# Performance work log

Measured on AMD Instinct MI355X. Metric: run time of the kernel, lower is better.

The kernel has to match this reference:

```python
import jax, jax.numpy as jnp
import numpy as np

D_MODEL = 2048
NUM_HEADS = 16
D_H = D_MODEL // NUM_HEADS
D_LATENT = 512
B, S = 2, 2048


def setup_inputs() -> dict:
    key = jax.random.key(0)
    ks = jax.random.split(key, 10)
    sd = lambda fan_in: 1.0 / np.sqrt(fan_in)
    x = jax.random.normal(ks[0], (B, S, D_MODEL), dtype=jnp.float32)
    # weights stored as [in, out] so y = x @ W + b (same math as nn.Linear)
    w_latent = jax.random.uniform(ks[1], (D_MODEL, D_LATENT), jnp.float32, -sd(D_MODEL), sd(D_MODEL))
    b_latent = jax.random.uniform(ks[2], (D_LATENT,), jnp.float32, -sd(D_MODEL), sd(D_MODEL))
    w_q = jax.random.uniform(ks[3], (D_MODEL, D_MODEL), jnp.float32, -sd(D_MODEL), sd(D_MODEL))
    b_q = jax.random.uniform(ks[4], (D_MODEL,), jnp.float32, -sd(D_MODEL), sd(D_MODEL))
    # per-head K/V projections batched into [H, d_latent, d_h]
    w_k = jax.random.uniform(ks[5], (NUM_HEADS, D_LATENT, D_H), jnp.float32, -sd(D_LATENT), sd(D_LATENT))
    b_k = jax.random.uniform(ks[6], (NUM_HEADS, D_H), jnp.float32, -sd(D_LATENT), sd(D_LATENT))
    w_v = jax.random.uniform(ks[7], (NUM_HEADS, D_LATENT, D_H), jnp.float32, -sd(D_LATENT), sd(D_LATENT))
    b_v = jax.random.uniform(ks[8], (NUM_HEADS, D_H), jnp.float32, -sd(D_LATENT), sd(D_LATENT))
    w_o = jax.random.uniform(ks[9], (D_MODEL, D_MODEL), jnp.float32, -sd(D_MODEL), sd(D_MODEL))
    b_o = jnp.zeros((D_MODEL,), jnp.float32)
    return {"x": x, "w_latent": w_latent, "b_latent": b_latent, "w_q": w_q, "b_q": b_q,
            "w_k": w_k, "b_k": b_k, "w_v": w_v, "b_v": b_v, "w_o": w_o, "b_o": b_o}


def reference(x, w_latent, b_latent, w_q, b_q, w_k, b_k, w_v, b_v, w_o, b_o):
    batch, seq, d = x.shape
    # latent KV compression: [B,S,d_latent]
    z = x @ w_latent + b_latent
    # queries: [B,H,S,d_h]
    q = (x @ w_q + b_q).reshape(batch, seq, NUM_HEADS, D_H).transpose(0, 2, 1, 3)
    # per-head K/V projections fused into one batched GEMM: [B,H,S,d_h]
    k = jnp.einsum('bsl,hld->bhsd', z, w_k) + b_k[None, :, None, :]
    v = jnp.einsum('bsl,hld->bhsd', z, w_v) + b_v[None, :, None, :]
    attn = jnp.einsum('bhqd,bhkd->bhqk', q, k) / np.sqrt(D_H).astype(np.float32)
    attn = jax.nn.softmax(attn, axis=-1)
    out = jnp.einsum('bhqk,bhkd->bhqd', attn, v)          # [B,H,S,d_h]
    out = out.transpose(0, 2, 1, 3).reshape(batch, seq, d)  # [B,S,D]
    return out @ w_o + b_o
```

## Files before the change

### kernel.cpp

```cpp
#include <hip/hip_runtime.h>
#include <hip/hip_bf16.h>

#define H_ATT   16
#define DH      128
#define DMODEL  2048
#define DLAT    512
#define NB      2
#define SEQ     2048
#define MROWS   (NB * SEQ)
#define NQZ     (DMODEL + DLAT)
#define NKV     (2 * DMODEL)

#define SCL2 0.12751744f

typedef __bf16          bf16x8_t __attribute__((ext_vector_type(8)));
typedef float           f32x4_t  __attribute__((ext_vector_type(4)));
typedef unsigned short  u16x4_t  __attribute__((ext_vector_type(4)));

#if __has_builtin(__builtin_amdgcn_exp2f)
#define EXP2F(x) __builtin_amdgcn_exp2f(x)
#else
#define EXP2F(x) exp2f(x)
#endif

__device__ __forceinline__ unsigned short f2bf_u16(float f) {
  union { __bf16 b; unsigned short u; } cv; cv.b = (__bf16)f; return cv.u;
}

__device__ __forceinline__ void async_copy16(const __bf16* g, __bf16* l) {
  __builtin_amdgcn_global_load_lds(
      (const __attribute__((address_space(1))) unsigned int*)g,
      (__attribute__((address_space(3))) unsigned int*)l, 16, 0, 0);
}

#define NB_CAST 8192
#define NB_WQ   4096
#define NB_WL   1024
#define NB_WK   1024
#define NB_WV   1024
#define NB_WO   4096
#define NB_BIAS 26
#define NB_PREP (NB_CAST + NB_WQ + NB_WL + NB_WK + NB_WV + NB_WO + NB_BIAS)

__global__ void prep(const float* __restrict__ x,
                     const float* __restrict__ w_q, const float* __restrict__ w_latent,
                     const float* __restrict__ w_k, const float* __restrict__ w_v,
                     const float* __restrict__ w_o,
                     const float* __restrict__ b_q, const float* __restrict__ b_lat,
                     const float* __restrict__ b_k, const float* __restrict__ b_v,
                     __bf16* __restrict__ xb, __bf16* __restrict__ wqzt,
                     __bf16* __restrict__ wkvt, __bf16* __restrict__ wot,
                     float* __restrict__ bqz, float* __restrict__ bkv) {
  __shared__ float tile[32][33];
  int bi = blockIdx.x;
  int t  = threadIdx.x;

  if (bi < NB_CAST) {
    int i = bi * 256 + t;
    float4 v = ((const float4*)x)[i];
    ushort4 o;
    o.x = f2bf_u16(v.x); o.y = f2bf_u16(v.y); o.z = f2bf_u16(v.z); o.w = f2bf_u16(v.w);
    ((ushort4*)xb)[i] = o;
    return;
  }
  bi -= NB_CAST;

  const float* in = nullptr; __bf16* out = nullptr;
  int R = 0, C = 0, bx = 0, by = 0; float scale = 1.f;
  if (bi < NB_WQ) {
    in = w_q; out = wqzt; R = DMODEL; C = DMODEL; scale = SCL2;
    bx = bi & 63; by = bi >> 6;
  } else if ((bi -= NB_WQ) < NB_WL) {
    in = w_latent; out = wqzt + (size_t)DMODEL * DMODEL; R = DMODEL; C = DLAT;
    bx = bi & 15; by = bi >> 4;
  } else if ((bi -= NB_WL) < NB_WK) {
    int h = bi >> 6, rem = bi & 63;
    in = w_k + (size_t)h * DLAT * DH; out = wkvt + (size_t)h * DH * DLAT;
    R = DLAT; C = DH; bx = rem & 3; by = rem >> 2;
  } else if ((bi -= NB_WK) < NB_WV) {
    int h = bi >> 6, rem = bi & 63;
    in = w_v + (size_t)h * DLAT * DH;
    out = wkvt + (size_t)DMODEL * DLAT + (size_t)h * DH * DLAT;
    R = DLAT; C = DH; bx = rem & 3; by = rem >> 2;
  } else if ((bi -= NB_WV) < NB_WO) {
    in = w_o; out = wot; R = DMODEL; C = DMODEL;
    bx = bi & 63; by = bi >> 6;
  } else {
    bi -= NB_WO;
    int idx = bi * 256 + t;
    if (idx < DMODEL)                bqz[idx] = b_q[idx] * SCL2;
    else if (idx < NQZ)              bqz[idx] = b_lat[idx - DMODEL];
    else if (idx < NQZ + DMODEL)     bkv[idx - NQZ] = b_k[idx - NQZ];
    else if (idx < NQZ + NKV)        bkv[idx - NQZ] = b_v[idx - NQZ - DMODEL];
    return;
  }

  int tx = t & 31, ty = t >> 5;
  const float* ip = in + (size_t)(by * 32) * C + bx * 32;
  #pragma unroll
  for (int i = 0; i < 4; ++i)
    tile[ty + i * 8][tx] = ip[(size_t)(ty + i * 8) * C + tx];
  __syncthreads();
  __bf16* op = out + (size_t)(bx * 32) * R + by * 32;
  #pragma unroll
  for (int i = 0; i < 4; ++i)
    op[(size_t)(ty + i * 8) * R + tx] = (__bf16)(tile[tx][ty + i * 8] * scale);
}

#define BM 128
#define BN 128
#define BK 32

__device__ __forceinline__ void storec(float*  p, float v) { *p = v; }
__device__ __forceinline__ void storec(__bf16* p, float v) { *p = (__bf16)v; }

template <typename OutT, bool KVDUAL>
__global__ __launch_bounds__(256, 2)
void gemm_bt(const __bf16* __restrict__ A, const __bf16* __restrict__ Bt,
             const float* __restrict__ bias, OutT* __restrict__ C,
             __bf16* __restrict__ Cvt,
             int M, int N, int K, int lda, int ldc) {
  __shared__ __align__(16) __bf16 As[BM * BK];
  __shared__ __align__(16) __bf16 Bs[BN * BK];
  const int t    = threadIdx.x;
  const int wave = t >> 6, lane = t & 63;
  const int quad = lane >> 4, l16 = lane & 15;
  const int wm = (wave >> 1) * 64, wn = (wave & 1) * 64;
  const int row0 = blockIdx.y * BM, col0 = blockIdx.x * BN;
  const int srow = t >> 2, skc = t & 3;

  const __bf16* Ag  = A  + (size_t)(row0 + srow)      * lda + skc * 8;
  const __bf16* Ag2 = A  + (size_t)(row0 + srow + 64) * lda + skc * 8;
  const __bf16* Bg  = Bt + (size_t)(col0 + srow)      * K   + skc * 8;
  const __bf16* Bg2 = Bt + (size_t)(col0 + srow + 64) * K   + skc * 8;
  __bf16* Al  = As + t * 8;
  __bf16* Al2 = As + 2048 + t * 8;
  __bf16* Bl  = Bs + t * 8;
  __bf16* Bl2 = Bs + 2048 + t * 8;

  f32x4_t acc[4][4] = {};

  for (int k0 = 0; k0 < K; k0 += BK) {
    async_copy16(Ag  + k0, Al);
    async_copy16(Ag2 + k0, Al2);
    async_copy16(Bg  + k0, Bl);
    async_copy16(Bg2 + k0, Bl2);
    __syncthreads();
    bf16x8_t af[4], bfr[4];
    #pragma unroll
    for (int i = 0; i < 4; ++i)
      af[i] = *(const bf16x8_t*)(As + (wm + i * 16 + l16) * BK + quad * 8);
    #pragma unroll
    for (int j = 0; j < 4; ++j)
      bfr[j] = *(const bf16x8_t*)(Bs + (wn + j * 16 + l16) * BK + quad * 8);
    #pragma unroll
    for (int i = 0; i < 4; ++i)
      #pragma unroll
      for (int j = 0; j < 4; ++j)
        acc[i][j] = __builtin_amdgcn_mfma_f32_16x16x32_bf16(af[i], bfr[j], acc[i][j], 0, 0, 0);
    __syncthreads();
  }

  const bool vmode = KVDUAL && (col0 >= DMODEL);
  #pragma unroll
  for (int j = 0; j < 4; ++j) {
    int col = col0 + wn + j * 16 + l16;
    float bj = bias[col];
    #pragma unroll
    for (int i = 0; i < 4; ++i) {
      int row = row0 + wm + i * 16 + quad * 4;
      if (vmode) {
        u16x4_t pw;
        #pragma unroll
        for (int r = 0; r < 4; ++r) pw[r] = f2bf_u16(acc[i][j][r] + bj);
        size_t bb = (size_t)(row >> 11);
        int s = row & (SEQ - 1);
        *(u16x4_t*)(Cvt + bb * ((size_t)DMODEL * SEQ) + (size_t)(col - DMODEL) * SEQ + s) = pw;
      } else {
        #pragma unroll
        for (int r = 0; r < 4; ++r)
          storec(&C[(size_t)(row + r) * ldc + col], acc[i][j][r] + bj);
      }
    }
  }
}

#define TQ 128
#define TK 64

__global__ __launch_bounds__(256, 2)
void mla_attn(const __bf16* __restrict__ Qm, const __bf16* __restrict__ Km,
              const __bf16* __restrict__ Vtg, __bf16* __restrict__ Om) {
  __shared__ __align__(16) __bf16 Kls[16 * 512];
  __shared__ __align__(16) __bf16 Vls[2][16 * 512];
  __shared__ __align__(16) __bf16 Ps [16 * 512];
  __shared__ float Lbuf[2][TQ];

  const int t    = threadIdx.x;
  const int wave = t >> 6, lane = t & 63;
  const int quad = lane >> 4, l16 = lane & 15;
  const int wq = wave >> 1, wk = wave & 1, wd = wave & 1;
  const int lin  = blockIdx.x;
  const int xcd  = lin & 7, slot = lin >> 3;
  const int hb   = xcd * 4 + (slot >> 4);
  const int b    = hb >> 4, h = hb & 15;
  const int q0   = (slot & 15) * TQ;
  const size_t kbase  = (size_t)b * SEQ * DMODEL + (size_t)h * DH;
  const size_t vtbase = ((size_t)b * DMODEL + (size_t)h * DH) * SEQ;
  const size_t obase  = (size_t)b * SEQ * DMODEL + (size_t)h * DH;

  bf16x8_t qf[4][4];
  #pragma unroll
  for (int nt = 0; nt < 4; ++nt) {
    const __bf16* qp = Qm + ((size_t)b * SEQ + q0 + wq * 64 + nt * 16 + l16) * NQZ
                       + (size_t)h * DH + quad * 8;
    #pragma unroll
    for (int kc = 0; kc < 4; ++kc)
      qf[nt][kc] = *(const bf16x8_t*)(qp + kc * 32);
  }

  auto stage = [&](int kt0, int vbuf) {
    #pragma unroll
    for (int i2 = 0; i2 < 4; ++i2) {
      int bidx = wave * 4 + i2;
      int mt = bidx >> 2, kc = bidx & 3;
      async_copy16(Km + kbase + (size_t)(kt0 + mt * 16 + l16) * DMODEL + kc * 32 + quad * 8,
                   Kls + bidx * 512 + lane * 8);
      int dt = bidx >> 1, ks = bidx & 1;
      async_copy16(Vtg + vtbase + (size_t)(dt * 16 + l16) * SEQ + kt0 + ks * 32 + quad * 8,
                   Vls[vbuf] + bidx * 512 + lane * 8);
    }
  };

  f32x4_t acc_o[4][4] = {};
  float l_part[4] = {0.f, 0.f, 0.f, 0.f};

  stage(0, 0);

  f32x4_t acc_s[2][4];
  for (int it = 0; it < SEQ / TK; ++it) {
    __syncthreads();

    if (it > 0) {
      const __bf16* Vb = Vls[(it - 1) & 1];
      #pragma unroll
      for (int ks = 0; ks < 2; ++ks) {
        bf16x8_t pf[4];
        #pragma unroll
        for (int mq = 0; mq < 4; ++mq)
          pf[mq] = *(const bf16x8_t*)(Ps + ((wq * 4 + mq) * 2 + ks) * 512 + lane * 8);
        #pragma unroll
        for (int nd = 0; nd < 4; ++nd) {
          bf16x8_t vf = *(const bf16x8_t*)(Vb + ((wd * 4 + nd) * 2 + ks) * 512 + lane * 8);
          #pragma unroll
          for (int mq = 0; mq < 4; ++mq)
            acc_o[mq][nd] = __builtin_amdgcn_mfma_f32_16x16x32_bf16(pf[mq], vf, acc_o[mq][nd], 0, 0, 0);
        }
      }
    }

    #pragma unroll
    for (int mtl = 0; mtl < 2; ++mtl)
      #pragma unroll
      for (int nt = 0; nt < 4; ++nt)
        acc_s[mtl][nt] = f32x4_t{0.f, 0.f, 0.f, 0.f};
    #pragma unroll
    for (int kc = 0; kc < 4; ++kc)
      #pragma unroll
      for (int mtl = 0; mtl < 2; ++mtl) {
        bf16x8_t kf = *(const bf16x8_t*)(Kls + ((wk * 2 + mtl) * 4 + kc) * 512 + lane * 8);
        #pragma unroll
        for (int nt = 0; nt < 4; ++nt)
          acc_s[mtl][nt] = __builtin_amdgcn_mfma_f32_16x16x32_bf16(kf, qf[nt][kc], acc_s[mtl][nt], 0, 0, 0);
      }

    __syncthreads();

    if (it + 1 < SEQ / TK) stage((it + 1) * TK, (it + 1) & 1);

    #pragma unroll
    for (int nt = 0; nt < 4; ++nt) {
      #pragma unroll
      for (int mtl = 0; mtl < 2; ++mtl) {
        u16x4_t pw;
        float s = 0.f;
        #pragma unroll
        for (int r = 0; r < 4; ++r) {
          float p = EXP2F(fminf(acc_s[mtl][nt][r], 80.f));
          s += p;
          pw[r] = f2bf_u16(p);
        }
        l_part[nt] += s;
        *(u16x4_t*)(Ps + ((wq * 4 + nt) * 2 + wk) * 512
                    + ((mtl * 2 + (quad >> 1)) * 16 + l16) * 8 + (quad & 1) * 4) = pw;
      }
    }
  }

  __syncthreads();
  {
    const __bf16* Vb = Vls[(SEQ / TK - 1) & 1];
    #pragma unroll
    for (int ks = 0; ks < 2; ++ks) {
      bf16x8_t pf[4];
      #pragma unroll
      for (int mq = 0; mq < 4; ++mq)
        pf[mq] = *(const bf16x8_t*)(Ps + ((wq * 4 + mq) * 2 + ks) * 512 + lane * 8);
      #pragma unroll
      for (int nd = 0; nd < 4; ++nd) {
        bf16x8_t vf = *(const bf16x8_t*)(Vb + ((wd * 4 + nd) * 2 + ks) * 512 + lane * 8);
        #pragma unroll
        for (int mq = 0; mq < 4; ++mq)
          acc_o[mq][nd] = __builtin_amdgcn_mfma_f32_16x16x32_bf16(pf[mq], vf, acc_o[mq][nd], 0, 0, 0);
      }
    }
  }

  #pragma unroll
  for (int nt = 0; nt < 4; ++nt) {
    float lp = l_part[nt];
    lp += __shfl_xor(lp, 16);
    lp += __shfl_xor(lp, 32);
    Lbuf[wk][wq * 64 + nt * 16 + l16] = lp;
  }
  __syncthreads();
  #pragma unroll
  for (int mq = 0; mq < 4; ++mq) {
    float li[4];
    #pragma unroll
    for (int r = 0; r < 4; ++r) {
      int qq = wq * 64 + mq * 16 + quad * 4 + r;
      li[r] = 1.f / (Lbuf[0][qq] + Lbuf[1][qq]);
    }
    #pragma unroll
    for (int nd = 0; nd < 4; ++nd) {
      int col = wd * 64 + nd * 16 + l16;
      #pragma unroll
      for (int r = 0; r < 4; ++r) {
        int row = q0 + wq * 64 + mq * 16 + quad * 4 + r;
        Om[obase + (size_t)row * DMODEL + col] = (__bf16)(acc_o[mq][nd][r] * li[r]);
      }
    }
  }
}

extern "C" void kernel_launch(void* const* d_in, const int* in_sizes, int n_in,
                              void* d_out, int out_size, void* d_ws, size_t ws_size,
                              hipStream_t stream) {
  (void)in_sizes; (void)n_in; (void)out_size; (void)ws_size;
  const float* x        = (const float*)d_in[0];
  const float* w_latent = (const float*)d_in[1];
  const float* b_latent = (const float*)d_in[2];
  const float* w_q      = (const float*)d_in[3];
  const float* b_q      = (const float*)d_in[4];
  const float* w_k      = (const float*)d_in[5];
  const float* b_k      = (const float*)d_in[6];
  const float* w_v      = (const float*)d_in[7];
  const float* b_v      = (const float*)d_in[8];
  const float* w_o      = (const float*)d_in[9];
  const float* b_o      = (const float*)d_in[10];
  float* out = (float*)d_out;

  __bf16* ws = (__bf16*)d_ws;
  __bf16* xb   = ws; ws += (size_t)MROWS * DMODEL;
  __bf16* wqzt = ws; ws += (size_t)NQZ * DMODEL;
  __bf16* wkvt = ws; ws += (size_t)NKV * DLAT;
  __bf16* wot  = ws; ws += (size_t)DMODEL * DMODEL;
  __bf16* qzb  = ws; ws += (size_t)MROWS * NQZ;
  __bf16* kb   = ws; ws += (size_t)MROWS * DMODEL;
  __bf16* vt   = ws; ws += (size_t)MROWS * DMODEL;
  __bf16* ao   = ws; ws += (size_t)MROWS * DMODEL;
  float*  bqz  = (float*)ws;
  float*  bkv  = bqz + NQZ;

  dim3 blk256(256);
  prep<<<NB_PREP, blk256, 0, stream>>>(x, w_q, w_latent, w_k, w_v, w_o,
                                       b_q, b_latent, b_k, b_v,
                                       xb, wqzt, wkvt, wot, bqz, bkv);

  gemm_bt<__bf16, false><<<dim3(NQZ/BN, MROWS/BM), blk256, 0, stream>>>(
      xb, wqzt, bqz, qzb, nullptr, MROWS, NQZ, DMODEL, DMODEL, NQZ);
  gemm_bt<__bf16, true><<<dim3(NKV/BN, MROWS/BM), blk256, 0, stream>>>(
      qzb + DMODEL, wkvt, bkv, kb, vt, MROWS, NKV, DLAT, NQZ, DMODEL);

  mla_attn<<<dim3(512), blk256, 0, stream>>>(qzb, kb, vt, ao);

  gemm_bt<float, false><<<dim3(DMODEL/BN, MROWS/BM), blk256, 0, stream>>>(
      ao, wot, b_o, out, nullptr, MROWS, DMODEL, DMODEL, DMODEL, DMODEL);
}
```

Measured before the change: 348.2 us.

## Double-buffer K tiles, split K/V staging, add MFMA priority hints in attention

The attention kernel now double-buffers the K tile as well as V. It issues the next K prefetch at the top of each iteration and the V prefetch after the score MFMAs, and replaces the second __syncthreads with a bare s_barrier. The MFMA sections are wrapped in s_setprio to favour matrix issue, and shared memory is merged into one aliased buffer, with Lbuf reusing the K region at the end. The GEMM launch bound is raised to 3 blocks per CU, which may force register spills. The bare barrier does not wait on outstanding memory operations, so correctness depends on the async-copy waits elsewhere.

```diff
diff --git a/kernel.cpp b/kernel.cpp
--- a/kernel.cpp
+++ b/kernel.cpp
@@ -115,7 +115,7 @@
 __device__ __forceinline__ void storec(__bf16* p, float v) { *p = (__bf16)v; }
 
 template <typename OutT, bool KVDUAL>
-__global__ __launch_bounds__(256, 2)
+__global__ __launch_bounds__(256, 3)
 void gemm_bt(const __bf16* __restrict__ A, const __bf16* __restrict__ Bt,
              const float* __restrict__ bias, OutT* __restrict__ C,
              __bf16* __restrict__ Cvt,
@@ -187,14 +187,16 @@
 
 #define TQ 128
 #define TK 64
+#define NT (SEQ / TK)
 
 __global__ __launch_bounds__(256, 2)
 void mla_attn(const __bf16* __restrict__ Qm, const __bf16* __restrict__ Km,
               const __bf16* __restrict__ Vtg, __bf16* __restrict__ Om) {
-  __shared__ __align__(16) __bf16 Kls[16 * 512];
-  __shared__ __align__(16) __bf16 Vls[2][16 * 512];
-  __shared__ __align__(16) __bf16 Ps [16 * 512];
-  __shared__ float Lbuf[2][TQ];
+  __shared__ __align__(16) __bf16 smem[5 * 16 * 512];
+  __bf16* const Kls = smem;
+  __bf16* const Vls = smem + 2 * (16 * 512);
+  __bf16* const Ps  = smem + 4 * (16 * 512);
+  float*  const Lbuf = (float*)smem;
 
   const int t    = threadIdx.x;
   const int wave = t >> 6, lane = t & 63;
@@ -219,30 +221,40 @@
       qf[nt][kc] = *(const bf16x8_t*)(qp + kc * 32);
   }
 
-  auto stage = [&](int kt0, int vbuf) {
+  auto stageK = [&](int kt0, int buf) {
     #pragma unroll
     for (int i2 = 0; i2 < 4; ++i2) {
       int bidx = wave * 4 + i2;
       int mt = bidx >> 2, kc = bidx & 3;
       async_copy16(Km + kbase + (size_t)(kt0 + mt * 16 + l16) * DMODEL + kc * 32 + quad * 8,
-                   Kls + bidx * 512 + lane * 8);
+                   Kls + buf * (16 * 512) + bidx * 512 + lane * 8);
+    }
+  };
+  auto stageV = [&](int kt0, int buf) {
+    #pragma unroll
+    for (int i2 = 0; i2 < 4; ++i2) {
+      int bidx = wave * 4 + i2;
       int dt = bidx >> 1, ks = bidx & 1;
       async_copy16(Vtg + vtbase + (size_t)(dt * 16 + l16) * SEQ + kt0 + ks * 32 + quad * 8,
-                   Vls[vbuf] + bidx * 512 + lane * 8);
+                   Vls + buf * (16 * 512) + bidx * 512 + lane * 8);
     }
   };
 
   f32x4_t acc_o[4][4] = {};
   float l_part[4] = {0.f, 0.f, 0.f, 0.f};
 
-  stage(0, 0);
+  stageK(0, 0);
+  stageV(0, 0);
 
   f32x4_t acc_s[2][4];
-  for (int it = 0; it < SEQ / TK; ++it) {
+  for (int it = 0; it < NT; ++it) {
     __syncthreads();
 
+    if (it + 1 < NT) stageK((it + 1) * TK, (it + 1) & 1);
+
     if (it > 0) {
-      const __bf16* Vb = Vls[(it - 1) & 1];
+      const __bf16* Vb = Vls + ((it - 1) & 1) * (16 * 512);
+      __builtin_amdgcn_s_setprio(1);
       #pragma unroll
       for (int ks = 0; ks < 2; ++ks) {
         bf16x8_t pf[4];
@@ -257,6 +269,7 @@
             acc_o[mq][nd] = __builtin_amdgcn_mfma_f32_16x16x32_bf16(pf[mq], vf, acc_o[mq][nd], 0, 0, 0);
         }
       }
+      __builtin_amdgcn_s_setprio(0);
     }
 
     #pragma unroll
@@ -264,19 +277,22 @@
       #pragma unroll
       for (int nt = 0; nt < 4; ++nt)
         acc_s[mtl][nt] = f32x4_t{0.f, 0.f, 0.f, 0.f};
+    const __bf16* Kb = Kls + (it & 1) * (16 * 512);
+    __builtin_amdgcn_s_setprio(1);
     #pragma unroll
     for (int kc = 0; kc < 4; ++kc)
       #pragma unroll
       for (int mtl = 0; mtl < 2; ++mtl) {
-        bf16x8_t kf = *(const bf16x8_t*)(Kls + ((wk * 2 + mtl) * 4 + kc) * 512 + lane * 8);
+        bf16x8_t kf = *(const bf16x8_t*)(Kb + ((wk * 2 + mtl) * 4 + kc) * 512 + lane * 8);
         #pragma unroll
         for (int nt = 0; nt < 4; ++nt)
           acc_s[mtl][nt] = __builtin_amdgcn_mfma_f32_16x16x32_bf16(kf, qf[nt][kc], acc_s[mtl][nt], 0, 0, 0);
       }
-
-    __syncthreads();
-
-    if (it + 1 < SEQ / TK) stage((it + 1) * TK, (it + 1) & 1);
+    __builtin_amdgcn_s_setprio(0);
+
+    __builtin_amdgcn_s_barrier();
+
+    if (it + 1 < NT) stageV((it + 1) * TK, (it + 1) & 1);
 
     #pragma unroll
     for (int nt = 0; nt < 4; ++nt) {
@@ -299,7 +315,8 @@
 
   __syncthreads();
   {
-    const __bf16* Vb = Vls[(SEQ / TK - 1) & 1];
+    const __bf16* Vb = Vls + ((NT - 1) & 1) * (16 * 512);
+    __builtin_amdgcn_s_setprio(1);
     #pragma unroll
     for (int ks = 0; ks < 2; ++ks) {
       bf16x8_t pf[4];
@@ -314,6 +331,7 @@
           acc_o[mq][nd] = __builtin_amdgcn_mfma_f32_16x16x32_bf16(pf[mq], vf, acc_o[mq][nd], 0, 0, 0);
       }
     }
+    __builtin_amdgcn_s_setprio(0);
   }
 
   #pragma unroll
@@ -321,7 +339,7 @@
     float lp = l_part[nt];
     lp += __shfl_xor(lp, 16);
     lp += __shfl_xor(lp, 32);
-    Lbuf[wk][wq * 64 + nt * 16 + l16] = lp;
+    Lbuf[wk * TQ + wq * 64 + nt * 16 + l16] = lp;
   }
   __syncthreads();
   #pragma unroll
@@ -330,7 +348,7 @@
     #pragma unroll
     for (int r = 0; r < 4; ++r) {
       int qq = wq * 64 + mq * 16 + quad * 4 + r;
-      li[r] = 1.f / (Lbuf[0][qq] + Lbuf[1][qq]);
+      li[r] = 1.f / (Lbuf[0 * TQ + qq] + Lbuf[1 * TQ + qq]);
     }
     #pragma unroll
     for (int nd = 0; nd < 4; ++nd) {
```

New measurement: 340.5 us. 1.02x faster.
